# Optimization experiments

Measured on AMD Instinct MI355X. Metric: run time of the kernel, lower is better.

The kernel has to match this reference:

```python
import jax, jax.numpy as jnp
import numpy as np

D = 2048
N_HEAD = 16
D_HEAD = D // N_HEAD
EXP = 4
EPS = 1e-6


def setup_inputs() -> dict:
    key = jax.random.key(0)
    ks = jax.random.split(key, 8)
    b, s = 2, 2048
    scale = 0.02
    return {
        "x": jax.random.normal(ks[0], (b, s, D), dtype=jnp.float32),
        "w_qkv": jax.random.normal(ks[1], (D, 3 * D), dtype=jnp.float32) * scale,
        "w_o": jax.random.normal(ks[2], (D, D), dtype=jnp.float32) * scale,
        "w_up": jax.random.normal(ks[3], (D, EXP * D), dtype=jnp.float32) * scale,
        "w_gate": jax.random.normal(ks[4], (D, EXP * D), dtype=jnp.float32) * scale,
        "w_down": jax.random.normal(ks[5], (EXP * D, D), dtype=jnp.float32) * scale,
        "scale1": jnp.ones((D,), dtype=jnp.float32),
        "scale2": jnp.ones((D,), dtype=jnp.float32),
    }


def _rmsnorm(x, scale):
    rms = jnp.sqrt(jnp.mean(x * x, axis=-1, keepdims=True) + EPS)
    return x / rms * scale


def _attention(x, w_qkv, w_o):
    b, s, d = x.shape
    qkv = x @ w_qkv  # [b, s, 3d]
    q, k, v = jnp.split(qkv, 3, axis=-1)
    # [b, h, s, dh]
    q = q.reshape(b, s, N_HEAD, D_HEAD).transpose(0, 2, 1, 3)
    k = k.reshape(b, s, N_HEAD, D_HEAD).transpose(0, 2, 1, 3)
    v = v.reshape(b, s, N_HEAD, D_HEAD).transpose(0, 2, 1, 3)
    scores = jnp.einsum("bhqd,bhkd->bhqk", q, k) / np.sqrt(D_HEAD).astype(np.float32)
    causal = jnp.tril(jnp.ones((s, s), dtype=bool))
    scores = jnp.where(causal, scores, -jnp.inf)
    attn = jax.nn.softmax(scores, axis=-1)
    out = jnp.einsum("bhqk,bhkd->bhqd", attn, v)
    out = out.transpose(0, 2, 1, 3).reshape(b, s, d)
    return out @ w_o


def _mlp(x, w_up, w_gate, w_down):
    return (x @ w_up * jax.nn.silu(x @ w_gate)) @ w_down


def reference(x, w_qkv, w_o, w_up, w_gate, w_down, scale1, scale2):
    x = x + _attention(_rmsnorm(x, scale1), w_qkv, w_o)
    x = x + _mlp(_rmsnorm(x, scale2), w_up, w_gate, w_down)
    return x
```

## Files before the change

kernel.cpp:

```cpp
#include <hip/hip_runtime.h>

typedef unsigned short u16;
typedef __bf16 bfrag8 __attribute__((ext_vector_type(8)));
typedef float f32x4 __attribute__((ext_vector_type(4)));

#define MFMA16(a, b, c) __builtin_amdgcn_mfma_f32_16x16x32_bf16((a), (b), (c), 0, 0, 0)

static __device__ __forceinline__ u16 bf_bits(float f) {
  unsigned int u = __builtin_bit_cast(unsigned int, f);
  unsigned int r = (u + 0x7fffu + ((u >> 16) & 1u)) >> 16;
  return (u16)r;
}
static __device__ __forceinline__ float f_from_bits(u16 u) {
  unsigned int w = ((unsigned int)u) << 16;
  return __builtin_bit_cast(float, w);
}
static __device__ __forceinline__ void gload16(const void* g, void* l) {
  __builtin_amdgcn_global_load_lds(
      (const __attribute__((address_space(1))) void*)g,
      (__attribute__((address_space(3))) void*)l, 16, 0, 0);
}

__global__ __launch_bounds__(256) void k_transpose_bf16(const float* __restrict__ src,
                                                        u16* __restrict__ dst,
                                                        int K, int N) {
  __shared__ float tile[32][33];
  const int n0 = blockIdx.x * 32;
  const int k0 = blockIdx.y * 32;
  const int t = threadIdx.x;
  const int lr = t >> 5;
  const int lc = t & 31;
#pragma unroll
  for (int i = 0; i < 4; ++i)
    tile[lr + i * 8][lc] = src[(size_t)(k0 + lr + i * 8) * N + n0 + lc];
  __syncthreads();
#pragma unroll
  for (int i = 0; i < 4; ++i)
    dst[(size_t)(n0 + lr + i * 8) * K + k0 + lc] = bf_bits(tile[lc][lr + i * 8]);
}

__global__ __launch_bounds__(256) void k_transpose_v(const u16* __restrict__ qkv,
                                                     u16* __restrict__ vtg) {
  __shared__ u16 tile[32][33];
  const int bh = blockIdx.z, b = bh >> 4, hh = bh & 15;
  const int s0 = blockIdx.x * 32, d0 = blockIdx.y * 32;
  const int t = threadIdx.x;
  const int lr = t >> 5, lc = t & 31;
#pragma unroll
  for (int i = 0; i < 4; ++i)
    tile[lr + i * 8][lc] =
        qkv[(size_t)(b * 2048 + s0 + lr + i * 8) * 6144 + 4096 + hh * 128 + d0 + lc];
  __syncthreads();
#pragma unroll
  for (int i = 0; i < 4; ++i)
    vtg[(size_t)bh * 128 * 2048 + (size_t)(d0 + lr + i * 8) * 2048 + s0 + lc] =
        tile[lc][lr + i * 8];
}

__global__ __launch_bounds__(256) void k_rmsnorm(const float* __restrict__ x,
                                                 const float* __restrict__ sc,
                                                 u16* __restrict__ o) {
  const int row = blockIdx.x;
  const int t = threadIdx.x;
  const float4* x4 = (const float4*)(x + (size_t)row * 2048);
  float4 a = x4[t];
  float4 b = x4[t + 256];
  float ss = a.x * a.x + a.y * a.y + a.z * a.z + a.w * a.w +
             b.x * b.x + b.y * b.y + b.z * b.z + b.w * b.w;
#pragma unroll
  for (int off = 32; off > 0; off >>= 1) ss += __shfl_down(ss, off);
  __shared__ float red[4];
  if ((t & 63) == 0) red[t >> 6] = ss;
  __syncthreads();
  const float inv = rsqrtf((red[0] + red[1] + red[2] + red[3]) * (1.0f / 2048.0f) + 1e-6f);
  const float4* s4 = (const float4*)sc;
  float4 sa = s4[t], sb = s4[t + 256];
  ushort4 pa, pb;
  pa.x = bf_bits(a.x * inv * sa.x); pa.y = bf_bits(a.y * inv * sa.y);
  pa.z = bf_bits(a.z * inv * sa.z); pa.w = bf_bits(a.w * inv * sa.w);
  pb.x = bf_bits(b.x * inv * sb.x); pb.y = bf_bits(b.y * inv * sb.y);
  pb.z = bf_bits(b.z * inv * sb.z); pb.w = bf_bits(b.w * inv * sb.w);
  *(ushort4*)(o + (size_t)row * 2048 + t * 4) = pa;
  *(ushort4*)(o + (size_t)row * 2048 + (t + 256) * 4) = pb;
}

template <int EPI, int K>
__global__ __launch_bounds__(256, 4) void k_gemm(const u16* __restrict__ A,
                                                 const u16* __restrict__ Bt,
                                                 int M, int N,
                                                 float* __restrict__ outF,
                                                 u16* __restrict__ outB,
                                                 const float* __restrict__ resid,
                                                 const u16* __restrict__ gate) {
  __shared__ u16 sm[16384];
  char* smC = (char*)sm;
  const int nbx = gridDim.x;
  const int f = blockIdx.x + nbx * blockIdx.y;
  const int nsl = nbx >> 3;
  const int x = f & 7;
  const int j = f >> 3;
  const int n0 = (x * nsl + (j % nsl)) * 128;
  const int m0 = (j / nsl) * 128;

  const int t = threadIdx.x;
  const int wid = t >> 6, lane = t & 63;
  const int wm = wid >> 1, wn = wid & 1;
  const int l15 = lane & 15, lhi = lane >> 4;
  const int lhi16 = lhi * 16;
  const int swz = (l15 & 7) << 4;

  f32x4 acc[4][4];
#pragma unroll
  for (int i = 0; i < 4; ++i)
#pragma unroll
    for (int j2 = 0; j2 < 4; ++j2) acc[i][j2] = (f32x4){0.f, 0.f, 0.f, 0.f};

  const int sr = lane >> 3;
  const int csw = (((lane & 7) * 16) ^ (sr << 4)) >> 1;
  const u16* Asrc = A + (size_t)(m0 + wid * 32 + sr) * K + csw;
  const u16* Bsrc = Bt + (size_t)(n0 + wid * 32 + sr) * K + csw;
  char* adst = smC + wid * 4096 + lane * 16;
  char* bdst = smC + 16384 + wid * 4096 + lane * 16;

  for (int kt = 0; kt < K / 64; ++kt) {
    __syncthreads();
    const u16* as = Asrc + kt * 64;
    const u16* bs = Bsrc + kt * 64;
#pragma unroll
    for (int c = 0; c < 4; ++c) {
      gload16(as + (size_t)c * 8 * K, adst + c * 1024);
      gload16(bs + (size_t)c * 8 * K, bdst + c * 1024);
    }
    asm volatile("s_waitcnt vmcnt(0)" ::: "memory");
    __syncthreads();

#pragma unroll
    for (int kh = 0; kh < 2; ++kh) {
      bfrag8 a0 = *(const bfrag8*)(smC + (wm * 64 + 0 * 16 + l15) * 128 + ((kh * 64 + lhi16) ^ swz));
      bfrag8 a1 = *(const bfrag8*)(smC + (wm * 64 + 1 * 16 + l15) * 128 + ((kh * 64 + lhi16) ^ swz));
      bfrag8 a2 = *(const bfrag8*)(smC + (wm * 64 + 2 * 16 + l15) * 128 + ((kh * 64 + lhi16) ^ swz));
      bfrag8 a3 = *(const bfrag8*)(smC + (wm * 64 + 3 * 16 + l15) * 128 + ((kh * 64 + lhi16) ^ swz));
      bfrag8 b0 = *(const bfrag8*)(smC + 16384 + (wn * 64 + 0 * 16 + l15) * 128 + ((kh * 64 + lhi16) ^ swz));
      bfrag8 b1 = *(const bfrag8*)(smC + 16384 + (wn * 64 + 1 * 16 + l15) * 128 + ((kh * 64 + lhi16) ^ swz));
      bfrag8 b2 = *(const bfrag8*)(smC + 16384 + (wn * 64 + 2 * 16 + l15) * 128 + ((kh * 64 + lhi16) ^ swz));
      bfrag8 b3 = *(const bfrag8*)(smC + 16384 + (wn * 64 + 3 * 16 + l15) * 128 + ((kh * 64 + lhi16) ^ swz));
      acc[0][0] = MFMA16(a0, b0, acc[0][0]); acc[0][1] = MFMA16(a0, b1, acc[0][1]);
      acc[0][2] = MFMA16(a0, b2, acc[0][2]); acc[0][3] = MFMA16(a0, b3, acc[0][3]);
      acc[1][0] = MFMA16(a1, b0, acc[1][0]); acc[1][1] = MFMA16(a1, b1, acc[1][1]);
      acc[1][2] = MFMA16(a1, b2, acc[1][2]); acc[1][3] = MFMA16(a1, b3, acc[1][3]);
      acc[2][0] = MFMA16(a2, b0, acc[2][0]); acc[2][1] = MFMA16(a2, b1, acc[2][1]);
      acc[2][2] = MFMA16(a2, b2, acc[2][2]); acc[2][3] = MFMA16(a2, b3, acc[2][3]);
      acc[3][0] = MFMA16(a3, b0, acc[3][0]); acc[3][1] = MFMA16(a3, b1, acc[3][1]);
      acc[3][2] = MFMA16(a3, b2, acc[3][2]); acc[3][3] = MFMA16(a3, b3, acc[3][3]);
    }
  }

#pragma unroll
  for (int i = 0; i < 4; ++i) {
#pragma unroll
    for (int j2 = 0; j2 < 4; ++j2) {
      const int mr = m0 + wm * 64 + i * 16 + lhi * 4;
      const int nc = n0 + wn * 64 + j2 * 16 + l15;
#pragma unroll
      for (int r = 0; r < 4; ++r) {
        const size_t idx = (size_t)(mr + r) * N + nc;
        const float v = acc[i][j2][r];
        if (EPI == 0) {
          outB[idx] = bf_bits(v);
        } else if (EPI == 1) {
          outF[idx] = resid[idx] + v;
        } else {
          float g = f_from_bits(gate[idx]);
          float s = g / (1.f + __expf(-g));
          outB[idx] = bf_bits(v * s);
        }
      }
    }
  }
}

template <int K>
__global__ __launch_bounds__(256, 2) void k_gemm_mlp(const u16* __restrict__ A,
                                                     const u16* __restrict__ Bg,
                                                     const u16* __restrict__ Bu,
                                                     int N,
                                                     u16* __restrict__ outB) {
  __shared__ u16 sm[24576];
  char* smC = (char*)sm;
  const int nbx = gridDim.x;
  const int f = blockIdx.x + nbx * blockIdx.y;
  const int nsl = nbx >> 3;
  const int x = f & 7;
  const int j = f >> 3;
  const int n0 = (x * nsl + (j % nsl)) * 128;
  const int m0 = (j / nsl) * 128;

  const int t = threadIdx.x;
  const int wid = t >> 6, lane = t & 63;
  const int wm = wid >> 1, wn = wid & 1;
  const int l15 = lane & 15, lhi = lane >> 4;
  const int lhi16 = lhi * 16;
  const int swz = (l15 & 7) << 4;

  f32x4 accg[4][4], accu[4][4];
#pragma unroll
  for (int i = 0; i < 4; ++i)
#pragma unroll
    for (int j2 = 0; j2 < 4; ++j2) {
      accg[i][j2] = (f32x4){0.f, 0.f, 0.f, 0.f};
      accu[i][j2] = (f32x4){0.f, 0.f, 0.f, 0.f};
    }

  const int sr = lane >> 3;
  const int csw = (((lane & 7) * 16) ^ (sr << 4)) >> 1;
  const u16* Asrc = A + (size_t)(m0 + wid * 32 + sr) * K + csw;
  const u16* Bgsrc = Bg + (size_t)(n0 + wid * 32 + sr) * K + csw;
  const u16* Busrc = Bu + (size_t)(n0 + wid * 32 + sr) * K + csw;
  char* adst = smC + wid * 4096 + lane * 16;
  char* bgdst = smC + 16384 + wid * 4096 + lane * 16;
  char* budst = smC + 32768 + wid * 4096 + lane * 16;

  for (int kt = 0; kt < K / 64; ++kt) {
    __syncthreads();
    const u16* as = Asrc + kt * 64;
    const u16* gs = Bgsrc + kt * 64;
    const u16* us = Busrc + kt * 64;
#pragma unroll
    for (int c = 0; c < 4; ++c) {
      gload16(as + (size_t)c * 8 * K, adst + c * 1024);
      gload16(gs + (size_t)c * 8 * K, bgdst + c * 1024);
      gload16(us + (size_t)c * 8 * K, budst + c * 1024);
    }
    asm volatile("s_waitcnt vmcnt(0)" ::: "memory");
    __syncthreads();

#pragma unroll
    for (int kh = 0; kh < 2; ++kh) {
      const int ko = (kh * 64 + lhi16);
      bfrag8 a0 = *(const bfrag8*)(smC + (wm * 64 + 0 * 16 + l15) * 128 + (ko ^ swz));
      bfrag8 a1 = *(const bfrag8*)(smC + (wm * 64 + 1 * 16 + l15) * 128 + (ko ^ swz));
      bfrag8 a2 = *(const bfrag8*)(smC + (wm * 64 + 2 * 16 + l15) * 128 + (ko ^ swz));
      bfrag8 a3 = *(const bfrag8*)(smC + (wm * 64 + 3 * 16 + l15) * 128 + (ko ^ swz));
      bfrag8 g0 = *(const bfrag8*)(smC + 16384 + (wn * 64 + 0 * 16 + l15) * 128 + (ko ^ swz));
      bfrag8 g1 = *(const bfrag8*)(smC + 16384 + (wn * 64 + 1 * 16 + l15) * 128 + (ko ^ swz));
      bfrag8 g2 = *(const bfrag8*)(smC + 16384 + (wn * 64 + 2 * 16 + l15) * 128 + (ko ^ swz));
      bfrag8 g3 = *(const bfrag8*)(smC + 16384 + (wn * 64 + 3 * 16 + l15) * 128 + (ko ^ swz));
      accg[0][0] = MFMA16(a0, g0, accg[0][0]); accg[0][1] = MFMA16(a0, g1, accg[0][1]);
      accg[0][2] = MFMA16(a0, g2, accg[0][2]); accg[0][3] = MFMA16(a0, g3, accg[0][3]);
      accg[1][0] = MFMA16(a1, g0, accg[1][0]); accg[1][1] = MFMA16(a1, g1, accg[1][1]);
      accg[1][2] = MFMA16(a1, g2, accg[1][2]); accg[1][3] = MFMA16(a1, g3, accg[1][3]);
      accg[2][0] = MFMA16(a2, g0, accg[2][0]); accg[2][1] = MFMA16(a2, g1, accg[2][1]);
      accg[2][2] = MFMA16(a2, g2, accg[2][2]); accg[2][3] = MFMA16(a2, g3, accg[2][3]);
      accg[3][0] = MFMA16(a3, g0, accg[3][0]); accg[3][1] = MFMA16(a3, g1, accg[3][1]);
      accg[3][2] = MFMA16(a3, g2, accg[3][2]); accg[3][3] = MFMA16(a3, g3, accg[3][3]);
      bfrag8 u0 = *(const bfrag8*)(smC + 32768 + (wn * 64 + 0 * 16 + l15) * 128 + (ko ^ swz));
      bfrag8 u1 = *(const bfrag8*)(smC + 32768 + (wn * 64 + 1 * 16 + l15) * 128 + (ko ^ swz));
      bfrag8 u2 = *(const bfrag8*)(smC + 32768 + (wn * 64 + 2 * 16 + l15) * 128 + (ko ^ swz));
      bfrag8 u3 = *(const bfrag8*)(smC + 32768 + (wn * 64 + 3 * 16 + l15) * 128 + (ko ^ swz));
      accu[0][0] = MFMA16(a0, u0, accu[0][0]); accu[0][1] = MFMA16(a0, u1, accu[0][1]);
      accu[0][2] = MFMA16(a0, u2, accu[0][2]); accu[0][3] = MFMA16(a0, u3, accu[0][3]);
      accu[1][0] = MFMA16(a1, u0, accu[1][0]); accu[1][1] = MFMA16(a1, u1, accu[1][1]);
      accu[1][2] = MFMA16(a1, u2, accu[1][2]); accu[1][3] = MFMA16(a1, u3, accu[1][3]);
      accu[2][0] = MFMA16(a2, u0, accu[2][0]); accu[2][1] = MFMA16(a2, u1, accu[2][1]);
      accu[2][2] = MFMA16(a2, u2, accu[2][2]); accu[2][3] = MFMA16(a2, u3, accu[2][3]);
      accu[3][0] = MFMA16(a3, u0, accu[3][0]); accu[3][1] = MFMA16(a3, u1, accu[3][1]);
      accu[3][2] = MFMA16(a3, u2, accu[3][2]); accu[3][3] = MFMA16(a3, u3, accu[3][3]);
    }
  }

#pragma unroll
  for (int i = 0; i < 4; ++i) {
#pragma unroll
    for (int j2 = 0; j2 < 4; ++j2) {
      const int mr = m0 + wm * 64 + i * 16 + lhi * 4;
      const int nc = n0 + wn * 64 + j2 * 16 + l15;
#pragma unroll
      for (int r = 0; r < 4; ++r) {
        const float g = accg[i][j2][r];
        const float u = accu[i][j2][r];
        const float s = g / (1.f + __expf(-g));
        outB[(size_t)(mr + r) * N + nc] = bf_bits(u * s);
      }
    }
  }
}

__global__ __launch_bounds__(512) void k_attn(const u16* __restrict__ qkv,
                                              const u16* __restrict__ vtg,
                                              u16* __restrict__ out) {
  const int S = 2048, LD = 6144;
  const float scale = 0.0883883476483184405f;
  const int bh = blockIdx.y;
  const int b = bh >> 4, hh = bh & 15;
  const int qt = (b == 0) ? (15 - (int)blockIdx.x) : (int)blockIdx.x;
  const int t = threadIdx.x;
  const int wave = t >> 6, lane = t & 63;
  const int l15 = lane & 15, lhi = lane >> 4;
  const int lhi16 = lhi * 16;
  const int swz = (l15 & 7) << 4;

  __shared__ u16 Kt[64 * 128];
  __shared__ u16 Vt[128 * 64];
  __shared__ u16 Pl[8][16][72];
  char* KtC = (char*)Kt;
  char* VtC = (char*)Vt;

  const int qrow = qt * 128 + wave * 16 + l15;
  const size_t qoff = (size_t)(b * S + qrow) * LD + hh * 128 + lhi * 8;
  bfrag8 qf[4];
#pragma unroll
  for (int ks = 0; ks < 4; ++ks) qf[ks] = *(const bfrag8*)(qkv + qoff + ks * 32);

  f32x4 oacc[8];
#pragma unroll
  for (int j = 0; j < 8; ++j) oacc[j] = (f32x4){0.f, 0.f, 0.f, 0.f};
  float m_i[4], l_i[4];
#pragma unroll
  for (int r = 0; r < 4; ++r) { m_i[r] = -INFINITY; l_i[r] = 0.f; }

  const int q_my = qt * 128 + wave * 16 + lhi * 4;
  const int q_wave_last = qt * 128 + wave * 16 + 15;

  const int keyA = t >> 4, keyB = 32 + (t >> 4);
  const int oK = (t & 15) * 16;
  const int dA = t >> 3, dB = 64 + (t >> 3);
  const int oV = (t & 7) * 16;
  const u16* kbase = qkv + (size_t)(b * S) * LD + 2048 + hh * 128;
  const u16* vbase = vtg + (size_t)bh * 128 * S;
  const u16* ksrcA = kbase + (size_t)keyA * LD + ((oK ^ ((keyA & 7) << 4)) >> 1);
  const u16* ksrcB = kbase + (size_t)keyB * LD + ((oK ^ ((keyB & 7) << 4)) >> 1);
  const u16* vsrcA = vbase + (size_t)dA * S + ((oV ^ ((dA & 7) << 4)) >> 1);
  const u16* vsrcB = vbase + (size_t)dB * S + ((oV ^ ((dB & 7) << 4)) >> 1);
  const unsigned int ldso0 = wave * 1024 + lane * 16;
  const unsigned int ldso1 = 8192 + wave * 1024 + lane * 16;
  const size_t kstep = (size_t)64 * LD;

  const int kt_max = 2 * qt + 1;
  for (int kt = 0; kt <= kt_max; ++kt) {
    __syncthreads();
    gload16(ksrcA + (size_t)kt * kstep, KtC + ldso0);
    gload16(ksrcB + (size_t)kt * kstep, KtC + ldso1);
    gload16(vsrcA + kt * 64, VtC + ldso0);
    gload16(vsrcB + kt * 64, VtC + ldso1);
    __syncthreads();

    if (kt * 64 <= q_wave_last) {
      f32x4 sfr[4];
#pragma unroll
      for (int j = 0; j < 4; ++j) {
        sfr[j] = (f32x4){0.f, 0.f, 0.f, 0.f};
        const int krow = j * 16 + l15;
#pragma unroll
        for (int ks = 0; ks < 4; ++ks) {
          bfrag8 kf = *(const bfrag8*)(KtC + krow * 256 + ((ks * 64 + lhi16) ^ swz));
          sfr[j] = MFMA16(qf[ks], kf, sfr[j]);
        }
      }
      float sv[4][4], rmax[4];
#pragma unroll
      for (int r = 0; r < 4; ++r) rmax[r] = -INFINITY;
#pragma unroll
      for (int j = 0; j < 4; ++j) {
        const int key = kt * 64 + j * 16 + l15;
#pragma unroll
        for (int r = 0; r < 4; ++r) {
          float v = sfr[j][r] * scale;
          v = (key <= q_my + r) ? v : -INFINITY;
          sv[j][r] = v;
          rmax[r] = fmaxf(rmax[r], v);
        }
      }
#pragma unroll
      for (int r = 0; r < 4; ++r) {
        float v = rmax[r];
        v = fmaxf(v, __shfl_xor(v, 1));
        v = fmaxf(v, __shfl_xor(v, 2));
        v = fmaxf(v, __shfl_xor(v, 4));
        v = fmaxf(v, __shfl_xor(v, 8));
        rmax[r] = v;
      }
      float alpha[4], rsum[4];
#pragma unroll
      for (int r = 0; r < 4; ++r) {
        float mn = fmaxf(m_i[r], rmax[r]);
        alpha[r] = __expf(m_i[r] - mn);
        m_i[r] = mn;
        rsum[r] = 0.f;
      }
#pragma unroll
      for (int j = 0; j < 4; ++j) {
#pragma unroll
        for (int r = 0; r < 4; ++r) {
          float p = __expf(sv[j][r] - m_i[r]);
          rsum[r] += p;
          Pl[wave][lhi * 4 + r][j * 16 + l15] = bf_bits(p);
        }
      }
#pragma unroll
      for (int r = 0; r < 4; ++r) {
        float v = rsum[r];
        v += __shfl_xor(v, 1); v += __shfl_xor(v, 2);
        v += __shfl_xor(v, 4); v += __shfl_xor(v, 8);
        l_i[r] = l_i[r] * alpha[r] + v;
      }
#pragma unroll
      for (int j = 0; j < 8; ++j)
#pragma unroll
        for (int r = 0; r < 4; ++r) oacc[j][r] *= alpha[r];

#pragma unroll
      for (int ks2 = 0; ks2 < 2; ++ks2) {
        bfrag8 pf = *(const bfrag8*)&Pl[wave][l15][ks2 * 32 + lhi * 8];
#pragma unroll
        for (int j = 0; j < 8; ++j) {
          const int d = j * 16 + l15;
          bfrag8 vf = *(const bfrag8*)(VtC + d * 128 + ((ks2 * 64 + lhi16) ^ swz));
          oacc[j] = MFMA16(pf, vf, oacc[j]);
        }
      }
    }
  }

#pragma unroll
  for (int r = 0; r < 4; ++r) {
    const float inv = 1.f / l_i[r];
    const size_t tok = (size_t)b * S + qt * 128 + wave * 16 + lhi * 4 + r;
#pragma unroll
    for (int j = 0; j < 8; ++j)
      out[tok * 2048 + hh * 128 + j * 16 + l15] = bf_bits(oacc[j][r] * inv);
  }
}

extern "C" void kernel_launch(void* const* d_in, const int* in_sizes, int n_in,
                              void* d_out, int out_size, void* d_ws, size_t ws_size,
                              hipStream_t stream) {
  (void)in_sizes; (void)n_in; (void)out_size; (void)ws_size;
  const float* x      = (const float*)d_in[0];
  const float* w_qkv  = (const float*)d_in[1];
  const float* w_o    = (const float*)d_in[2];
  const float* w_up   = (const float*)d_in[3];
  const float* w_gate = (const float*)d_in[4];
  const float* w_down = (const float*)d_in[5];
  const float* scale1 = (const float*)d_in[6];
  const float* scale2 = (const float*)d_in[7];
  float* out = (float*)d_out;

  u16* B       = (u16*)d_ws;
  u16* wqkvT   = B;
  u16* woT     = wqkvT  + (size_t)6144 * 2048;
  u16* wgateT  = woT    + (size_t)2048 * 2048;
  u16* wupT    = wgateT + (size_t)8192 * 2048;
  u16* wdownT  = wupT   + (size_t)8192 * 2048;
  u16* xn      = wdownT + (size_t)2048 * 8192;
  u16* qkvb    = xn     + (size_t)4096 * 2048;
  u16* attnb   = qkvb   + (size_t)4096 * 6144;
  float* y1    = (float*)(attnb + (size_t)4096 * 2048);
  u16* vtg     = (u16*)y1;
  u16* hbuf    = qkvb;

  dim3 blk(256);
  k_transpose_bf16<<<dim3(192, 64), blk, 0, stream>>>(w_qkv,  wqkvT,  2048, 6144);
  k_transpose_bf16<<<dim3(64, 64),  blk, 0, stream>>>(w_o,    woT,    2048, 2048);
  k_transpose_bf16<<<dim3(256, 64), blk, 0, stream>>>(w_gate, wgateT, 2048, 8192);
  k_transpose_bf16<<<dim3(256, 64), blk, 0, stream>>>(w_up,   wupT,   2048, 8192);
  k_transpose_bf16<<<dim3(64, 256), blk, 0, stream>>>(w_down, wdownT, 8192, 2048);

  k_rmsnorm<<<4096, blk, 0, stream>>>(x, scale1, xn);
  k_gemm<0, 2048><<<dim3(48, 32), blk, 0, stream>>>(xn, wqkvT, 4096, 6144, nullptr, qkvb, nullptr, nullptr);
  k_transpose_v<<<dim3(64, 4, 32), blk, 0, stream>>>(qkvb, vtg);
  k_attn<<<dim3(16, 32), dim3(512), 0, stream>>>(qkvb, vtg, attnb);
  k_gemm<1, 2048><<<dim3(16, 32), blk, 0, stream>>>(attnb, woT, 4096, 2048, y1, nullptr, x, nullptr);
  k_rmsnorm<<<4096, blk, 0, stream>>>(y1, scale2, xn);
  k_gemm_mlp<2048><<<dim3(64, 32), blk, 0, stream>>>(xn, wgateT, wupT, 8192, hbuf);
  k_gemm<1, 8192><<<dim3(16, 32), blk, 0, stream>>>(hbuf, wdownT, 4096, 2048, out, nullptr, y1, nullptr);
}
```

Before: 865.4 us.

## Use two-wave 128x128 GEMM tiles and regroup MLP block-to-tile mapping

The generic GEMM now runs with 128 threads (two waves) per 128x128 tile. Each wave computes a 128x64 sub-tile with 32 accumulators, reusing its B fragments across eight A fragments, so per-wave LDS reads per MFMA drop. The MLP GEMM's block-to-tile swizzle is also reordered to group pairs of N tiles across all M rows, aiming at better L2 reuse of weights. The trade-offs are higher register pressure, fewer waves per CU to hide latency, and each wave issuing twice as many global-to-LDS loads.

```diff
diff --git a/kernel.cpp b/kernel.cpp
--- a/kernel.cpp
+++ b/kernel.cpp
@@ -85,7 +85,7 @@
 }
 
 template <int EPI, int K>
-__global__ __launch_bounds__(256, 4) void k_gemm(const u16* __restrict__ A,
+__global__ __launch_bounds__(128, 2) void k_gemm(const u16* __restrict__ A,
                                                  const u16* __restrict__ Bt,
                                                  int M, int N,
                                                  float* __restrict__ outF,
@@ -104,30 +104,29 @@
 
   const int t = threadIdx.x;
   const int wid = t >> 6, lane = t & 63;
-  const int wm = wid >> 1, wn = wid & 1;
   const int l15 = lane & 15, lhi = lane >> 4;
   const int lhi16 = lhi * 16;
   const int swz = (l15 & 7) << 4;
 
-  f32x4 acc[4][4];
-#pragma unroll
-  for (int i = 0; i < 4; ++i)
+  f32x4 acc[8][4];
+#pragma unroll
+  for (int i = 0; i < 8; ++i)
 #pragma unroll
     for (int j2 = 0; j2 < 4; ++j2) acc[i][j2] = (f32x4){0.f, 0.f, 0.f, 0.f};
 
   const int sr = lane >> 3;
   const int csw = (((lane & 7) * 16) ^ (sr << 4)) >> 1;
-  const u16* Asrc = A + (size_t)(m0 + wid * 32 + sr) * K + csw;
-  const u16* Bsrc = Bt + (size_t)(n0 + wid * 32 + sr) * K + csw;
-  char* adst = smC + wid * 4096 + lane * 16;
-  char* bdst = smC + 16384 + wid * 4096 + lane * 16;
+  const u16* Asrc = A + (size_t)(m0 + wid * 64 + sr) * K + csw;
+  const u16* Bsrc = Bt + (size_t)(n0 + wid * 64 + sr) * K + csw;
+  char* adst = smC + wid * 8192 + lane * 16;
+  char* bdst = smC + 16384 + wid * 8192 + lane * 16;
 
   for (int kt = 0; kt < K / 64; ++kt) {
     __syncthreads();
     const u16* as = Asrc + kt * 64;
     const u16* bs = Bsrc + kt * 64;
 #pragma unroll
-    for (int c = 0; c < 4; ++c) {
+    for (int c = 0; c < 8; ++c) {
       gload16(as + (size_t)c * 8 * K, adst + c * 1024);
       gload16(bs + (size_t)c * 8 * K, bdst + c * 1024);
     }
@@ -136,31 +135,28 @@
 
 #pragma unroll
     for (int kh = 0; kh < 2; ++kh) {
-      bfrag8 a0 = *(const bfrag8*)(smC + (wm * 64 + 0 * 16 + l15) * 128 + ((kh * 64 + lhi16) ^ swz));
-      bfrag8 a1 = *(const bfrag8*)(smC + (wm * 64 + 1 * 16 + l15) * 128 + ((kh * 64 + lhi16) ^ swz));
-      bfrag8 a2 = *(const bfrag8*)(smC + (wm * 64 + 2 * 16 + l15) * 128 + ((kh * 64 + lhi16) ^ swz));
-      bfrag8 a3 = *(const bfrag8*)(smC + (wm * 64 + 3 * 16 + l15) * 128 + ((kh * 64 + lhi16) ^ swz));
-      bfrag8 b0 = *(const bfrag8*)(smC + 16384 + (wn * 64 + 0 * 16 + l15) * 128 + ((kh * 64 + lhi16) ^ swz));
-      bfrag8 b1 = *(const bfrag8*)(smC + 16384 + (wn * 64 + 1 * 16 + l15) * 128 + ((kh * 64 + lhi16) ^ swz));
-      bfrag8 b2 = *(const bfrag8*)(smC + 16384 + (wn * 64 + 2 * 16 + l15) * 128 + ((kh * 64 + lhi16) ^ swz));
-      bfrag8 b3 = *(const bfrag8*)(smC + 16384 + (wn * 64 + 3 * 16 + l15) * 128 + ((kh * 64 + lhi16) ^ swz));
-      acc[0][0] = MFMA16(a0, b0, acc[0][0]); acc[0][1] = MFMA16(a0, b1, acc[0][1]);
-      acc[0][2] = MFMA16(a0, b2, acc[0][2]); acc[0][3] = MFMA16(a0, b3, acc[0][3]);
-      acc[1][0] = MFMA16(a1, b0, acc[1][0]); acc[1][1] = MFMA16(a1, b1, acc[1][1]);
-      acc[1][2] = MFMA16(a1, b2, acc[1][2]); acc[1][3] = MFMA16(a1, b3, acc[1][3]);
-      acc[2][0] = MFMA16(a2, b0, acc[2][0]); acc[2][1] = MFMA16(a2, b1, acc[2][1]);
-      acc[2][2] = MFMA16(a2, b2, acc[2][2]); acc[2][3] = MFMA16(a2, b3, acc[2][3]);
-      acc[3][0] = MFMA16(a3, b0, acc[3][0]); acc[3][1] = MFMA16(a3, b1, acc[3][1]);
-      acc[3][2] = MFMA16(a3, b2, acc[3][2]); acc[3][3] = MFMA16(a3, b3, acc[3][3]);
-    }
-  }
-
-#pragma unroll
-  for (int i = 0; i < 4; ++i) {
+      const int ko = kh * 64 + lhi16;
+      bfrag8 b0 = *(const bfrag8*)(smC + 16384 + (wid * 64 + 0 * 16 + l15) * 128 + (ko ^ swz));
+      bfrag8 b1 = *(const bfrag8*)(smC + 16384 + (wid * 64 + 1 * 16 + l15) * 128 + (ko ^ swz));
+      bfrag8 b2 = *(const bfrag8*)(smC + 16384 + (wid * 64 + 2 * 16 + l15) * 128 + (ko ^ swz));
+      bfrag8 b3 = *(const bfrag8*)(smC + 16384 + (wid * 64 + 3 * 16 + l15) * 128 + (ko ^ swz));
+#pragma unroll
+      for (int i = 0; i < 8; ++i) {
+        bfrag8 ai = *(const bfrag8*)(smC + (i * 16 + l15) * 128 + (ko ^ swz));
+        acc[i][0] = MFMA16(ai, b0, acc[i][0]);
+        acc[i][1] = MFMA16(ai, b1, acc[i][1]);
+        acc[i][2] = MFMA16(ai, b2, acc[i][2]);
+        acc[i][3] = MFMA16(ai, b3, acc[i][3]);
+      }
+    }
+  }
+
+#pragma unroll
+  for (int i = 0; i < 8; ++i) {
 #pragma unroll
     for (int j2 = 0; j2 < 4; ++j2) {
-      const int mr = m0 + wm * 64 + i * 16 + lhi * 4;
-      const int nc = n0 + wn * 64 + j2 * 16 + l15;
+      const int mr = m0 + i * 16 + lhi * 4;
+      const int nc = n0 + wid * 64 + j2 * 16 + l15;
 #pragma unroll
       for (int r = 0; r < 4; ++r) {
         const size_t idx = (size_t)(mr + r) * N + nc;
@@ -189,11 +185,13 @@
   char* smC = (char*)sm;
   const int nbx = gridDim.x;
   const int f = blockIdx.x + nbx * blockIdx.y;
-  const int nsl = nbx >> 3;
   const int x = f & 7;
   const int j = f >> 3;
-  const int n0 = (x * nsl + (j % nsl)) * 128;
-  const int m0 = (j / nsl) * 128;
+  const int ni = j & 1;
+  const int m = (j >> 1) & 31;
+  const int nb = j >> 6;
+  const int n0 = (x * 8 + nb * 2 + ni) * 128;
+  const int m0 = m * 128;
 
   const int t = threadIdx.x;
   const int wid = t >> 6, lane = t & 63;
@@ -466,11 +464,11 @@
   k_transpose_bf16<<<dim3(64, 256), blk, 0, stream>>>(w_down, wdownT, 8192, 2048);
 
   k_rmsnorm<<<4096, blk, 0, stream>>>(x, scale1, xn);
-  k_gemm<0, 2048><<<dim3(48, 32), blk, 0, stream>>>(xn, wqkvT, 4096, 6144, nullptr, qkvb, nullptr, nullptr);
+  k_gemm<0, 2048><<<dim3(48, 32), dim3(128), 0, stream>>>(xn, wqkvT, 4096, 6144, nullptr, qkvb, nullptr, nullptr);
   k_transpose_v<<<dim3(64, 4, 32), blk, 0, stream>>>(qkvb, vtg);
   k_attn<<<dim3(16, 32), dim3(512), 0, stream>>>(qkvb, vtg, attnb);
-  k_gemm<1, 2048><<<dim3(16, 32), blk, 0, stream>>>(attnb, woT, 4096, 2048, y1, nullptr, x, nullptr);
+  k_gemm<1, 2048><<<dim3(16, 32), dim3(128), 0, stream>>>(attnb, woT, 4096, 2048, y1, nullptr, x, nullptr);
   k_rmsnorm<<<4096, blk, 0, stream>>>(y1, scale2, xn);
   k_gemm_mlp<2048><<<dim3(64, 32), blk, 0, stream>>>(xn, wgateT, wupT, 8192, hbuf);
-  k_gemm<1, 8192><<<dim3(16, 32), blk, 0, stream>>>(hbuf, wdownT, 4096, 2048, out, nullptr, y1, nullptr);
-}
+  k_gemm<1, 8192><<<dim3(16, 32), dim3(128), 0, stream>>>(hbuf, wdownT, 4096, 2048, out, nullptr, y1, nullptr);
+}
```

Result: slower. 910.9 us (+5.3%).
